# Kernel tuning notes

Hardware: AMD Instinct MI355X
Metric: run time of the kernel (lower is better)

The kernel has to match this reference:

```python
import jax, jax.numpy as jnp
import numpy as np

# Orbital structure for basis {A: [2s, 2p, 1d]} -> full_basis l values
LS = [0, 0, 1, 1, 2]
DIMS = [2 * l + 1 for l in LS]            # [1,1,3,3,5]
OFFS = np.concatenate([[0], np.cumsum(DIMS)]).astype(int)
NORB = int(sum(DIMS))                      # 13

# Upper-triangular orbital-pair layout of the flat feature vector
PAIRS = []
_off = 0
for _i in range(len(LS)):
    for _j in range(_i, len(LS)):
        PAIRS.append((_i, _j, _off))
        _off += DIMS[_i] * DIMS[_j]
FEAT_DIM = _off                            # 107

N_ATOMS, N_EDGES, N_KPTS = 256, 4096, 4


def _assemble_blocks(feat):
    """[B, FEAT_DIM] -> [B, NORB, NORB], upper-tri orbital blocks, 0.5 on diagonal pairs."""
    B = feat.shape[0]
    blk = jnp.zeros((B, NORB, NORB), feat.dtype)
    for (i, j, o) in PAIRS:
        di, dj = DIMS[i], DIMS[j]
        f = 0.5 if i == j else 1.0
        blk = blk.at[:, OFFS[i]:OFFS[i] + di, OFFS[j]:OFFS[j] + dj].set(
            f * feat[:, o:o + di * dj].reshape(B, di, dj))
    return blk


def setup_inputs() -> dict:
    key = jax.random.key(0)
    k1, k2, k3, k4, k5 = jax.random.split(key, 5)
    return {
        "orbpair_hopping": jax.random.normal(k1, (N_EDGES, FEAT_DIM), jnp.float32),
        "orbpair_onsite": jax.random.normal(k2, (N_ATOMS, FEAT_DIM), jnp.float32),
        "kpoints": jax.random.uniform(k3, (N_KPTS, 3), jnp.float32),
        "edge_cell_shift": jax.random.randint(k4, (N_EDGES, 3), -3, 4).astype(jnp.float32),
        "edge_index": jax.random.randint(k5, (2, N_EDGES), 0, N_ATOMS),
    }


def reference(orbpair_hopping, orbpair_onsite, kpoints, edge_cell_shift, edge_index):
    hop = _assemble_blocks(orbpair_hopping)      # [E, norb, norb]
    onsite = _assemble_blocks(orbpair_onsite)    # [N, norb, norb]
    N, K = onsite.shape[0], kpoints.shape[0]
    cplx = jnp.complex64

    # phase[k, e] = exp(-i 2pi k . R_e)
    phase = jnp.exp(-2j * jnp.pi * (kpoints @ edge_cell_shift.T)).astype(cplx)  # [K, E]

    # H(k) in block form [K, N, N, norb, norb]
    blk = jnp.zeros((K, N, N, NORB, NORB), cplx)
    ar = jnp.arange(N)
    blk = blk.at[:, ar, ar].set(onsite.astype(cplx)[None])  # diagonal onsite blocks
    ei, ej = edge_index[0], edge_index[1]
    blk = blk.at[:, ei, ej].add(phase[:, :, None, None] * hop.astype(cplx)[None])

    H = blk.transpose(0, 1, 3, 2, 4).reshape(K, N * NORB, N * NORB)
    return H + jnp.conj(jnp.swapaxes(H, 1, 2))  # hermitianize
```

## Files before the change

### kernel.cpp

```cpp
#include <hip/hip_runtime.h>

#define NORB 13
#define FEAT 107
#define TWO_PI 6.28318530717958647692f
#define NN 3328
#define ROWF (NN * 2)
#define R4 (NN / 2)
#define EMAX 4096
#define CAP 128
#define MAXS 48

__device__ __forceinline__ void map_pq(int p, int q, int& idx, float& scl) {
    const int DIMS[5] = {1, 1, 3, 3, 5};
    const int OFFS[5] = {0, 1, 2, 5, 8};
    idx = -1; scl = 0.0f;
    int o = 0;
    #pragma unroll
    for (int i = 0; i < 5; ++i) {
        #pragma unroll
        for (int j = i; j < 5; ++j) {
            int di = DIMS[i], dj = DIMS[j];
            if (p >= OFFS[i] && p < OFFS[i] + di && q >= OFFS[j] && q < OFFS[j] + dj) {
                idx = o + (p - OFFS[i]) * dj + (q - OFFS[j]);
                scl = (i == j) ? 0.5f : 1.0f;
            }
            o += di * dj;
        }
    }
}

__global__ __launch_bounds__(256)
void mono_kernel(const float* __restrict__ hop, const float* __restrict__ ons,
                 const float* __restrict__ kpt, const float* __restrict__ shf,
                 const int* __restrict__ eidx, float* __restrict__ out, int E) {
    int z = blockIdx.x;
    int k = z >> 9;
    int a = (z >> 1) & 255;
    int half = z & 1;
    int rbase = half ? 7 : 0;
    int nrows = half ? 6 : 7;
    int t = threadIdx.x;

    __shared__ int ilist[CAP];
    __shared__ int nmatch;
    __shared__ float2 phl[CAP];
    __shared__ unsigned char present[256];
    __shared__ unsigned char smap[256];
    __shared__ unsigned long long wmask[4];
    __shared__ float2 pblk[MAXS][91];

    if (t == 0) nmatch = 0;
    present[t] = 0;
    __syncthreads();

    for (int e = t; e < E; e += 256) {
        int ei = eidx[e], ej = eidx[E + e];
        if (ei == a) { int s = atomicAdd(&nmatch, 1); if (s < CAP) ilist[s] = (ej << 13) | (e << 1); }
        if (ej == a) { int s = atomicAdd(&nmatch, 1); if (s < CAP) ilist[s] = (ei << 13) | (e << 1) | 1; }
    }
    __syncthreads();
    int n = nmatch;
    int nb = n < CAP ? n : CAP;

    for (int i = t; i < nb; i += 256) present[ilist[i] >> 13] = 1;
    if (t == 0) present[a] = 1;
    __syncthreads();

    float kx = kpt[k * 3], ky = kpt[k * 3 + 1], kz = kpt[k * 3 + 2];
    for (int i = t; i < nb; i += 256) {
        int e = (ilist[i] >> 1) & 4095;
        float th = -TWO_PI * (kx * shf[e * 3] + ky * shf[e * 3 + 1] + kz * shf[e * 3 + 2]);
        float s, c;
        __sincosf(th, &s, &c);
        phl[i] = make_float2(c, s);
    }

    unsigned long long m = __ballot(present[t] != 0);
    int w = t >> 6;
    if ((t & 63) == 0) wmask[w] = m;
    __syncthreads();
    int nslots = __popcll(wmask[0]) + __popcll(wmask[1]) +
                 __popcll(wmask[2]) + __popcll(wmask[3]);

    int nloc = nrows * 13;

    if (n <= CAP && nslots <= MAXS) {
        if (present[t]) {
            int pre = 0;
            #pragma unroll
            for (int i = 0; i < 4; ++i) if (i < w) pre += __popcll(wmask[i]);
            pre += __popcll(wmask[w] & ((1ull << (t & 63)) - 1ull));
            smap[t] = (unsigned char)pre;
        } else {
            smap[t] = 255;
        }
        __syncthreads();

        float2* pf = &pblk[0][0];
        for (int i = t; i < nslots * 91; i += 256) pf[i] = make_float2(0.f, 0.f);
        __syncthreads();

        if (t < nloc) {
            int p = rbase + t / 13, q = t % 13;
            int i0, i1; float s0, s1;
            map_pq(p, q, i0, s0);
            map_pq(q, p, i1, s1);
            {
                const float* f = ons + (long)a * FEAT;
                float v = 0.f;
                if (i0 >= 0) v += s0 * f[i0];
                if (i1 >= 0) v += s1 * f[i1];
                pblk[smap[a]][t].x += v;
            }
            for (int i = 0; i < nb; ++i) {
                int pk = ilist[i];
                int b = pk >> 13;
                int e = (pk >> 1) & 4095;
                int dir = pk & 1;
                float hv = dir ? ((i1 >= 0) ? s1 * hop[(long)e * FEAT + i1] : 0.f)
                               : ((i0 >= 0) ? s0 * hop[(long)e * FEAT + i0] : 0.f);
                float2 ph = phl[i];
                float2 v = pblk[smap[b]][t];
                v.x += ph.x * hv;
                v.y += (dir ? -ph.y : ph.y) * hv;
                pblk[smap[b]][t] = v;
            }
        }
        __syncthreads();

        float4* out4 = (float4*)out;
        for (int rr = 0; rr < nrows; ++rr) {
            long rowb = (long)(k * NN + a * 13 + rbase + rr) * R4;
            int rloc = rr * 13;
            for (int f = t; f < R4; f += 256) {
                int c0 = 2 * f, c1 = c0 + 1;
                int b0 = (unsigned)c0 / 13u;
                int b1 = (unsigned)c1 / 13u;
                int m0 = smap[b0], m1 = smap[b1];
                float4 v = make_float4(0.f, 0.f, 0.f, 0.f);
                if (m0 != 255) { float2 pv = pblk[m0][rloc + (c0 - 13 * b0)]; v.x = pv.x; v.y = pv.y; }
                if (m1 != 255) { float2 pv = pblk[m1][rloc + (c1 - 13 * b1)]; v.z = pv.x; v.w = pv.y; }
                out4[rowb + f] = v;
            }
        }
    } else {
        float4 z4 = make_float4(0.f, 0.f, 0.f, 0.f);
        float4* out4 = (float4*)out;
        for (int rr = 0; rr < nrows; ++rr) {
            long rowb = (long)(k * NN + a * 13 + rbase + rr) * R4;
            for (int f = t; f < R4; f += 256) out4[rowb + f] = z4;
        }
        __syncthreads();
        if (t < nloc) {
            int p = rbase + t / 13, q = t % 13;
            int i0, i1; float s0, s1;
            map_pq(p, q, i0, s0);
            map_pq(q, p, i1, s1);
            {
                const float* f = ons + (long)a * FEAT;
                float v = 0.f;
                if (i0 >= 0) v += s0 * f[i0];
                if (i1 >= 0) v += s1 * f[i1];
                long off = (long)(k * NN + a * 13 + p) * ROWF + (a * 13 + q) * 2;
                atomicAdd(&out[off], v);
            }
            if (n <= CAP) {
                for (int i = 0; i < nb; ++i) {
                    int pk = ilist[i];
                    int b = pk >> 13, e = (pk >> 1) & 4095, dir = pk & 1;
                    float hv = dir ? ((i1 >= 0) ? s1 * hop[(long)e * FEAT + i1] : 0.f)
                                   : ((i0 >= 0) ? s0 * hop[(long)e * FEAT + i0] : 0.f);
                    float2 ph = phl[i];
                    long off = (long)(k * NN + a * 13 + p) * ROWF + (b * 13 + q) * 2;
                    atomicAdd(&out[off], ph.x * hv);
                    atomicAdd(&out[off + 1], (dir ? -ph.y : ph.y) * hv);
                }
            } else {
                for (int e = 0; e < E; ++e) {
                    int ei = eidx[e], ej = eidx[E + e];
                    #pragma unroll
                    for (int dir = 0; dir < 2; ++dir) {
                        int sa = dir ? ej : ei, b = dir ? ei : ej;
                        if (sa != a) continue;
                        float hv = dir ? ((i1 >= 0) ? s1 * hop[(long)e * FEAT + i1] : 0.f)
                                       : ((i0 >= 0) ? s0 * hop[(long)e * FEAT + i0] : 0.f);
                        float th = -TWO_PI * (kx * shf[e*3] + ky * shf[e*3+1] + kz * shf[e*3+2]);
                        float s, c;
                        __sincosf(th, &s, &c);
                        long off = (long)(k * NN + a * 13 + p) * ROWF + (b * 13 + q) * 2;
                        atomicAdd(&out[off], c * hv);
                        atomicAdd(&out[off + 1], (dir ? -s : s) * hv);
                    }
                }
            }
        }
    }
}


__global__ void zero_kernel(float4* __restrict__ out, long n4) {
    long i = (long)blockIdx.x * blockDim.x + threadIdx.x;
    long stride = (long)gridDim.x * blockDim.x;
    float4 zz = make_float4(0.f, 0.f, 0.f, 0.f);
    for (; i < n4; i += stride) out[i] = zz;
}

template <int CPX>
__global__ void onsite_kernel(const float* __restrict__ onsite, float* __restrict__ out,
                              int K, long nn) {
    int a = blockIdx.x;
    int t = threadIdx.x;
    if (t >= NORB * NORB) return;
    int p = t / NORB, q = t % NORB;
    int i1, i2; float s1, s2;
    map_pq(p, q, i1, s1);
    map_pq(q, p, i2, s2);
    const float* f = onsite + (long)a * FEAT;
    float v = 0.0f;
    if (i1 >= 0) v += s1 * f[i1];
    if (i2 >= 0) v += s2 * f[i2];
    long row = (long)a * NORB + p;
    long col = (long)a * NORB + q;
    for (int k = 0; k < K; ++k) {
        long off = (((long)k * nn + row) * nn + col) * CPX;
        out[off] = v;
    }
}

template <int CPX>
__global__ void edge_kernel(const float* __restrict__ hop, const float* __restrict__ kpts,
                            const float* __restrict__ shift, const int* __restrict__ eidx,
                            float* __restrict__ out, int E, int K, long nn) {
    int e = blockIdx.x;
    int t = threadIdx.x;
    __shared__ float phc[16], phs[16];
    int ei = eidx[e];
    int ej = eidx[E + e];
    if (t < K && t < 16) {
        float rx = shift[(long)e * 3 + 0];
        float ry = shift[(long)e * 3 + 1];
        float rz = shift[(long)e * 3 + 2];
        float th = -TWO_PI * (kpts[t * 3 + 0] * rx + kpts[t * 3 + 1] * ry + kpts[t * 3 + 2] * rz);
        float s, c;
        __sincosf(th, &s, &c);
        phc[t] = c; phs[t] = s;
    }
    __syncthreads();
    if (t >= NORB * NORB) return;
    int p = t / NORB, q = t % NORB;
    int idx; float scl;
    map_pq(p, q, idx, scl);
    if (idx < 0) return;
    float v = scl * hop[(long)e * FEAT + idx];
    long r1 = (long)ei * NORB + p, c1 = (long)ej * NORB + q;
    long r2 = (long)ej * NORB + q, c2 = (long)ei * NORB + p;
    for (int k = 0; k < K; ++k) {
        float pr = phc[k], pi = phs[k];
        long o1 = (((long)k * nn + r1) * nn + c1) * CPX;
        long o2 = (((long)k * nn + r2) * nn + c2) * CPX;
        atomicAdd(&out[o1], pr * v);
        atomicAdd(&out[o2], pr * v);
        if (CPX == 2) {
            atomicAdd(&out[o1 + 1], pi * v);
            atomicAdd(&out[o2 + 1], -pi * v);
        }
    }
}


extern "C" void kernel_launch(void* const* d_in, const int* in_sizes, int n_in,
                              void* d_out, int out_size, void* d_ws, size_t ws_size,
                              hipStream_t stream) {
    const float* hop  = (const float*)d_in[0];
    const float* ons  = (const float*)d_in[1];
    const float* kpt  = (const float*)d_in[2];
    const float* shf  = (const float*)d_in[3];
    const int*   eidx = (const int*)d_in[4];

    int E = in_sizes[0] / FEAT;
    int N = in_sizes[1] / FEAT;
    int K = in_sizes[2] / 3;
    long nn = (long)N * NORB;

    float* out = (float*)d_out;
    long knn2 = (long)K * nn * nn * 2;

    bool fast = (N == 256) && (K == 4) && (E <= EMAX) &&
                ((long)out_size == knn2);

    if (fast) {
        mono_kernel<<<2048, 256, 0, stream>>>(hop, ons, kpt, shf, eidx, out, E);
    } else {
        int cpx = ((long)out_size >= knn2) ? 2 : 1;
        long n4 = (long)out_size / 4;
        zero_kernel<<<2048, 256, 0, stream>>>((float4*)out, n4);
        if (cpx == 2) {
            onsite_kernel<2><<<N, 192, 0, stream>>>(ons, out, K, nn);
            edge_kernel<2><<<E, 192, 0, stream>>>(hop, kpt, shf, eidx, out, E, K, nn);
        } else {
            onsite_kernel<1><<<N, 192, 0, stream>>>(ons, out, K, nn);
            edge_kernel<1><<<E, 192, 0, stream>>>(hop, kpt, shf, eidx, out, E, K, nn);
        }
    }
}
```

Measured before the change: 79.68 us.

## Split dense output fill into separate zero pass plus sparse block scatter

The fused kernel that wrote every output row (zeros plus nonzero blocks) is replaced by a standalone grid-stride zero kernel followed by a paint kernel that writes only the nonzero 13-column blocks for each present neighbor slot. A slot-to-atom table is added so the scatter can index blocks directly. The intent is a simpler streaming zero fill and a cheap sparse write, at the cost of an extra launch and a second, uncoalesced, partial pass over output rows.

```diff
diff --git a/kernel.cpp b/kernel.cpp
--- a/kernel.cpp
+++ b/kernel.cpp
@@ -29,10 +29,17 @@
     }
 }
 
+__global__ void zero_kernel(float4* __restrict__ out, long n4) {
+    long i = (long)blockIdx.x * blockDim.x + threadIdx.x;
+    long stride = (long)gridDim.x * blockDim.x;
+    float4 zz = make_float4(0.f, 0.f, 0.f, 0.f);
+    for (; i < n4; i += stride) out[i] = zz;
+}
+
 __global__ __launch_bounds__(256)
-void mono_kernel(const float* __restrict__ hop, const float* __restrict__ ons,
-                 const float* __restrict__ kpt, const float* __restrict__ shf,
-                 const int* __restrict__ eidx, float* __restrict__ out, int E) {
+void paint_kernel(const float* __restrict__ hop, const float* __restrict__ ons,
+                  const float* __restrict__ kpt, const float* __restrict__ shf,
+                  const int* __restrict__ eidx, float* __restrict__ out, int E) {
     int z = blockIdx.x;
     int k = z >> 9;
     int a = (z >> 1) & 255;
@@ -46,6 +53,7 @@
     __shared__ float2 phl[CAP];
     __shared__ unsigned char present[256];
     __shared__ unsigned char smap[256];
+    __shared__ unsigned char sblk[MAXS];
     __shared__ unsigned long long wmask[4];
     __shared__ float2 pblk[MAXS][91];
 
@@ -91,6 +99,7 @@
             for (int i = 0; i < 4; ++i) if (i < w) pre += __popcll(wmask[i]);
             pre += __popcll(wmask[w] & ((1ull << (t & 63)) - 1ull));
             smap[t] = (unsigned char)pre;
+            if (pre < MAXS) sblk[pre] = (unsigned char)t;
         } else {
             smap[t] = 255;
         }
@@ -128,29 +137,18 @@
         }
         __syncthreads();
 
-        float4* out4 = (float4*)out;
-        for (int rr = 0; rr < nrows; ++rr) {
-            long rowb = (long)(k * NN + a * 13 + rbase + rr) * R4;
-            int rloc = rr * 13;
-            for (int f = t; f < R4; f += 256) {
-                int c0 = 2 * f, c1 = c0 + 1;
-                int b0 = (unsigned)c0 / 13u;
-                int b1 = (unsigned)c1 / 13u;
-                int m0 = smap[b0], m1 = smap[b1];
-                float4 v = make_float4(0.f, 0.f, 0.f, 0.f);
-                if (m0 != 255) { float2 pv = pblk[m0][rloc + (c0 - 13 * b0)]; v.x = pv.x; v.y = pv.y; }
-                if (m1 != 255) { float2 pv = pblk[m1][rloc + (c1 - 13 * b1)]; v.z = pv.x; v.w = pv.y; }
-                out4[rowb + f] = v;
-            }
+        float2* out2 = (float2*)out;
+        int total = nslots * nloc;
+        for (int u = t; u < total; u += 256) {
+            int s = u / nloc;
+            int v = u - s * nloc;
+            int rr = v / 13;
+            int q = v - rr * 13;
+            int b = sblk[s];
+            long off = (long)(k * NN + a * 13 + rbase + rr) * NN + b * 13 + q;
+            out2[off] = pblk[s][v];
         }
     } else {
-        float4 z4 = make_float4(0.f, 0.f, 0.f, 0.f);
-        float4* out4 = (float4*)out;
-        for (int rr = 0; rr < nrows; ++rr) {
-            long rowb = (long)(k * NN + a * 13 + rbase + rr) * R4;
-            for (int f = t; f < R4; f += 256) out4[rowb + f] = z4;
-        }
-        __syncthreads();
         if (t < nloc) {
             int p = rbase + t / 13, q = t % 13;
             int i0, i1; float s0, s1;
@@ -198,13 +196,6 @@
 }
 
 
-__global__ void zero_kernel(float4* __restrict__ out, long n4) {
-    long i = (long)blockIdx.x * blockDim.x + threadIdx.x;
-    long stride = (long)gridDim.x * blockDim.x;
-    float4 zz = make_float4(0.f, 0.f, 0.f, 0.f);
-    for (; i < n4; i += stride) out[i] = zz;
-}
-
 template <int CPX>
 __global__ void onsite_kernel(const float* __restrict__ onsite, float* __restrict__ out,
                               int K, long nn) {
@@ -288,12 +279,13 @@
     bool fast = (N == 256) && (K == 4) && (E <= EMAX) &&
                 ((long)out_size == knn2);
 
+    long n4 = (long)out_size / 4;
+    zero_kernel<<<2048, 256, 0, stream>>>((float4*)out, n4);
+
     if (fast) {
-        mono_kernel<<<2048, 256, 0, stream>>>(hop, ons, kpt, shf, eidx, out, E);
+        paint_kernel<<<2048, 256, 0, stream>>>(hop, ons, kpt, shf, eidx, out, E);
     } else {
         int cpx = ((long)out_size >= knn2) ? 2 : 1;
-        long n4 = (long)out_size / 4;
-        zero_kernel<<<2048, 256, 0, stream>>>((float4*)out, n4);
         if (cpx == 2) {
             onsite_kernel<2><<<N, 192, 0, stream>>>(ons, out, K, nn);
             edge_kernel<2><<<E, 192, 0, stream>>>(hop, kpt, shf, eidx, out, E, K, nn);
```

New measurement: 80.49 us. No clear change (+1.0%).
